# Performance work log

Measured on AMD Instinct MI355X. Metric: run time of the kernel, lower is better.

## Reference

```python
import jax, jax.numpy as jnp
import numpy as np

B, NJ, NM = 64, 30, 20
N = NJ * NM          # 600 operation nodes per FJSP instance
IN_DIM, H = 2, 128


def _bn(h):
    # torch BatchNorm1d in training mode, gamma=1/beta=0 (module init), stats over all nodes
    m = h.mean(axis=(0, 1))
    v = h.var(axis=(0, 1))
    return (h - m) / jnp.sqrt(v + 1e-5)


def setup_inputs() -> dict:
    key = jax.random.key(0)
    ks = jax.random.split(key, 20)
    x = jax.random.normal(ks[0], (B, N, IN_DIM), jnp.float32)
    graph_pool = jnp.full((B, N), 1.0 / N, jnp.float32)   # average graph pooling weights
    padded_nei = jnp.zeros((1,), jnp.int32)               # unused (sum pooling path)
    adj = (jax.random.uniform(ks[1], (B, N, N)) < 0.01).astype(jnp.float32)
    adj = jnp.minimum(adj + jnp.eye(N, dtype=jnp.float32)[None], 1.0)  # self-loops
    candidate = jax.random.randint(ks[2], (B, NJ), 0, N)
    a_index = jax.random.randint(ks[3], (B,), 0, NJ)
    mask = jax.random.uniform(ks[4], (B, NJ)) < 0.2
    mask = mask.at[jnp.arange(B), a_index].set(False)     # chosen action never masked
    mask_mch = jax.random.uniform(ks[5], (B, N, NM)) < 0.3
    dur = jax.random.uniform(ks[6], (B, N, NM), dtype=jnp.float32)
    old_action = jax.random.randint(ks[7], (B,), 0, N)
    mch_pool = jax.random.normal(ks[8], (B, H), jnp.float32)

    def w(k, i, o):
        return jax.random.normal(k, (i, o), jnp.float32) * (1.0 / np.sqrt(i))

    z = lambda n: jnp.zeros((n,), jnp.float32)            # biases init to 0 in module
    return dict(
        x=x, graph_pool=graph_pool, padded_nei=padded_nei, adj=adj,
        candidate=candidate, mask=mask, mask_mch=mask_mch, dur=dur,
        a_index=a_index, old_action=old_action, mch_pool=mch_pool,
        W1_0=w(ks[9], IN_DIM, H), b1_0=z(H), W2_0=w(ks[10], H, H), b2_0=z(H),
        W1_1=w(ks[11], H, H), b1_1=z(H), W2_1=w(ks[12], H, H), b2_1=z(H),
        Wa1=w(ks[13], 3 * H, H), ba1=z(H), Wa2=w(ks[14], H, H), ba2=z(H),
        Wa3=w(ks[15], H, 1), ba3=z(1),
        Wc1=w(ks[16], H, H), bc1=z(H), Wc2=w(ks[17], H, 1), bc2=z(1),
    )


def reference(x, graph_pool, padded_nei, adj, candidate, mask, mask_mch, dur,
              a_index, old_action, mch_pool,
              W1_0, b1_0, W2_0, b2_0, W1_1, b1_1, W2_1, b2_1,
              Wa1, ba1, Wa2, ba2, Wa3, ba3, Wc1, bc1, Wc2, bc2):
    # --- GIN encoder: num_layers-1 = 2 message-passing layers, sum pooling ---
    h = x
    for (W1, b1, W2, b2) in ((W1_0, b1_0, W2_0, b2_0), (W1_1, b1_1, W2_1, b2_1)):
        pooled = jnp.einsum('bnm,bmd->bnd', adj, h)         # neighbor sum (adj has self-loops)
        h1 = jax.nn.relu(_bn(pooled @ W1 + b1))             # MLP hidden (BN inside MLP)
        h = jax.nn.relu(_bn(h1 @ W2 + b2))                  # layer BN + relu
    h_nodes = h                                             # [B, N, H]
    h_pooled = jnp.einsum('bn,bnd->bd', graph_pool, h_nodes)  # [B, H]

    # --- gather candidate features, concat pooled contexts ---
    cand_feat = jnp.take_along_axis(h_nodes, candidate[:, :, None], axis=1)  # [B, NJ, H]
    concat = jnp.concatenate([
        cand_feat,
        jnp.broadcast_to(h_pooled[:, None, :], cand_feat.shape),
        jnp.broadcast_to(mch_pool[:, None, :], cand_feat.shape)], axis=-1)   # [B, NJ, 3H]

    # --- MLPActor(3 layers, tanh) ---
    a = jnp.tanh(concat @ Wa1 + ba1)
    a = jnp.tanh(a @ Wa2 + ba2)
    scores = (a @ Wa3 + ba3).squeeze(-1) * 10.0             # [B, NJ]
    scores = jnp.where(mask, -jnp.inf, scores)
    logpi = jax.nn.log_softmax(scores, axis=1)
    pi = jnp.exp(logpi)
    log_a = jnp.take_along_axis(logpi, a_index[:, None], axis=1)[:, 0]
    entropy = -jnp.sum(jnp.where(pi > 0, pi * logpi, 0.0), axis=1)

    # --- gather action-dependent tensors (detached in torch) ---
    b_idx = jnp.arange(B)
    action_node = dur[b_idx, old_action]                    # [B, NM]
    action_feature = h_nodes[b_idx, old_action]             # [B, H]
    mask_mch_action = mask_mch[b_idx, old_action][:, None, :]  # [B, 1, NM]

    # --- MLPCritic(2 layers, tanh) ---
    v = jnp.tanh(h_pooled @ Wc1 + bc1) @ Wc2 + bc2          # [B, 1]

    sg = jax.lax.stop_gradient
    return (entropy, v, log_a, sg(action_node), sg(action_feature),
            mask_mch_action, sg(h_pooled))
```

## Files before the change

### kernel.cpp

```cpp
#include <hip/hip_runtime.h>
#include <hip/hip_bf16.h>

#define BB 64
#define NJ 30
#define NM 20
#define NN 600
#define HH 128
#define NROWS (BB*NN)
#define CAP 48

typedef __attribute__((ext_vector_type(8))) short short8;
typedef __attribute__((ext_vector_type(4))) float f32x4;

#define STATS_B   0
#define HPOOL_B   4096
#define FLAGS_B   36864
#define ZERO_B    36880
#define WTB_B     37120
#define SCORES_B  135424
#define NBRCNT_B  143104
#define NBRIDX_B  296704
#define POOLED0_B 7669504
#define T1_B      7976704
#define P1_B      27637504

#define OUT_ENT   0
#define OUT_V     64
#define OUT_LOGA  128
#define OUT_ANODE 192
#define OUT_AFEAT 1472
#define OUT_MMCH  9664
#define OUT_HPOOL 10944

__device__ __forceinline__ bool mask_at(const void* p, int layout, long i) {
    if (layout == 2) return ((const float*)p)[i] != 0.f;
    if (layout == 1) return ((const unsigned char*)p)[i] != 0;
    return ((const int*)p)[i] != 0;
}

__device__ __forceinline__ short bf16rne(float f) {
    unsigned u = __float_as_uint(f);
    return (short)((u + 0x7fffu + ((u >> 16) & 1u)) >> 16);
}
__device__ __forceinline__ float bf2f(unsigned h) {
    return __uint_as_float(h << 16);
}
__device__ __forceinline__ unsigned packbf(float a, float b) {
    return ((unsigned)(unsigned short)bf16rne(a)) |
           (((unsigned)(unsigned short)bf16rne(b)) << 16);
}

__global__ __launch_bounds__(256) void k_sparse(const float* __restrict__ adj,
                                                const float* __restrict__ x,
                                                int* __restrict__ nbr_cnt,
                                                int* __restrict__ nbr_idx,
                                                float* __restrict__ pooled0,
                                                const void* mask_p, const void* maskmch_p,
                                                int* flags,
                                                const float* __restrict__ Wa,
                                                const float* __restrict__ Wb,
                                                const float* __restrict__ Wc,
                                                unsigned short* __restrict__ wT) {
    int bid = blockIdx.x;
    int tid = threadIdx.x;
    if (bid < 289) {
        if (bid >= 97) {
            int bid2 = bid - 97;
            int mat = bid2 >> 6;
            int idx = ((bid2 & 63) << 8) + tid;
            const float* W = mat == 0 ? Wa : (mat == 1 ? Wb : Wc);
            int k = idx >> 7, c = idx & 127;
            wT[mat * 16384 + c * HH + k] = (unsigned short)bf16rne(W[idx]);
        } else {
            unsigned agg = 0;
            int which;
            if (bid == 0) {
                which = 0;
                const unsigned* p = (const unsigned*)mask_p;
                unsigned w0 = (tid < 480) ? p[tid] : 0u;
                unsigned w1 = (tid + 256 < 480) ? p[tid + 256] : 0u;
                agg = w0 | w1;
            } else {
                which = 1;
                const unsigned* p = (const unsigned*)maskmch_p + (size_t)(bid - 1) * 200;
                agg = (tid < 200) ? p[tid] : 0u;
            }
            int f = 0;
            if (((agg >> 24) & 0xffu) == 0x3fu) f |= 1;
            if ((((agg >> 8) & 0xffu) == 1u) || (((agg >> 16) & 0xffu) == 1u) ||
                (((agg >> 24) & 0xffu) == 1u)) f |= 2;
#pragma unroll
            for (int off = 1; off < 64; off <<= 1) f |= __shfl_xor(f, off);
            if ((tid & 63) == 0 && f) atomicOr(&flags[which], f);
        }
    }

    int wrow = bid * 4 + (tid >> 6);
    int lane = tid & 63;
    int b = wrow / NN;
    const float4* arow = (const float4*)(adj + (size_t)wrow * NN);
    int* irow = nbr_idx + (size_t)wrow * CAP;
    const float* xb = x + (size_t)b * NN * 2;
    float4 vv[3];
    vv[0] = arow[lane];
    vv[1] = arow[64 + lane];
    vv[2] = (128 + lane < 150) ? arow[128 + lane] : make_float4(0.f, 0.f, 0.f, 0.f);
    int cnt = 0;
    float p0 = 0.f, p1 = 0.f;
#pragma unroll
    for (int it = 0; it < 3; ++it) {
        float4 v = vv[it];
        int col0 = it * 256 + lane * 4;
        bool m0 = v.x != 0.f, m1 = v.y != 0.f, m2 = v.z != 0.f, m3 = v.w != 0.f;
        int c_lane = (int)m0 + (int)m1 + (int)m2 + (int)m3;
        int inc = c_lane;
#pragma unroll
        for (int off = 1; off < 64; off <<= 1) {
            int t = __shfl_up(inc, off);
            if (lane >= off) inc += t;
        }
        int pos = cnt + inc - c_lane;
        if (m0) {
            if (pos < CAP) irow[pos] = col0;
            float2 xv = *(const float2*)&xb[col0 * 2];
            p0 += xv.x; p1 += xv.y; ++pos;
        }
        if (m1) {
            if (pos < CAP) irow[pos] = col0 + 1;
            float2 xv = *(const float2*)&xb[(col0 + 1) * 2];
            p0 += xv.x; p1 += xv.y; ++pos;
        }
        if (m2) {
            if (pos < CAP) irow[pos] = col0 + 2;
            float2 xv = *(const float2*)&xb[(col0 + 2) * 2];
            p0 += xv.x; p1 += xv.y; ++pos;
        }
        if (m3) {
            if (pos < CAP) irow[pos] = col0 + 3;
            float2 xv = *(const float2*)&xb[(col0 + 3) * 2];
            p0 += xv.x; p1 += xv.y; ++pos;
        }
        cnt += __shfl(inc, 63);
    }
#pragma unroll
    for (int off = 1; off < 64; off <<= 1) {
        p0 += __shfl_xor(p0, off);
        p1 += __shfl_xor(p1, off);
    }
    if (lane == 0) {
        nbr_cnt[wrow] = cnt < CAP ? cnt : CAP;
        pooled0[(size_t)wrow * 2]     = p0;
        pooled0[(size_t)wrow * 2 + 1] = p1;
    }
}

__global__ __launch_bounds__(256) void k_p0stats(const float* __restrict__ pooled0,
                                                 float* __restrict__ out5) {
    __shared__ float red[4][5];
    int i = blockIdx.x * 256 + threadIdx.x;
    float p0 = pooled0[(size_t)i * 2], p1 = pooled0[(size_t)i * 2 + 1];
    float v[5] = {p0, p1, p0 * p0, p1 * p1, p0 * p1};
#pragma unroll
    for (int j = 0; j < 5; ++j)
#pragma unroll
        for (int off = 1; off < 64; off <<= 1) v[j] += __shfl_xor(v[j], off);
    int lane = threadIdx.x & 63, w = threadIdx.x >> 6;
    if (lane == 0)
#pragma unroll
        for (int j = 0; j < 5; ++j) red[w][j] = v[j];
    __syncthreads();
    if (threadIdx.x == 0)
#pragma unroll
        for (int j = 0; j < 5; ++j)
            atomicAdd(&out5[j], red[0][j] + red[1][j] + red[2][j] + red[3][j]);
}

template<int MODE>
__global__ __launch_bounds__(256) void k_stage(const void* __restrict__ t_in_v,
                                               const float* __restrict__ pooled0,
                                               const float* __restrict__ W1,
                                               const unsigned short* __restrict__ wT,
                                               const float* __restrict__ stats_in,
                                               unsigned short* __restrict__ t_out,
                                               float* __restrict__ stats_out) {
    __shared__ float sm_mean[HH], sm_inv[HH];
    __shared__ float smS[4][32], smQ[4][32];
    int tid = threadIdx.x;
    if (MODE == 0 && tid < HH) {
        float S0 = stats_in[0], S1 = stats_in[1], Q0 = stats_in[2], Q1 = stats_in[3], P01 = stats_in[4];
        float w0 = W1[tid], w1 = W1[HH + tid];
        float m = (S0 * w0 + S1 * w1) * (1.f / NROWS);
        float eq = (Q0 * w0 * w0 + Q1 * w1 * w1 + 2.f * P01 * w0 * w1) * (1.f / NROWS);
        sm_mean[tid] = m;
        sm_inv[tid] = 1.f / sqrtf(eq - m * m + 1e-5f);
    }
    if (MODE == 1 && tid < HH) {
        float s = stats_in[tid], q = stats_in[HH + tid];
        float m = s * (1.f / NROWS);
        sm_mean[tid] = m;
        sm_inv[tid] = 1.f / sqrtf(q * (1.f / NROWS) - m * m + 1e-5f);
    }
    if (MODE != 2) __syncthreads();

    const unsigned short* tin = (const unsigned short*)t_in_v;
    int lane = tid & 63, wave = tid >> 6;
    int r16 = lane & 15, kg = lane >> 4;
    int rowbase = (blockIdx.x >> 2) * 64 + wave * 16;
    int colq = blockIdx.x & 3;

    f32x4 acc[2];
#pragma unroll
    for (int t = 0; t < 2; ++t)
#pragma unroll
        for (int i = 0; i < 4; ++i) acc[t][i] = 0.f;

    float p0 = 0.f, p1 = 0.f;
    if (MODE == 0) {
        p0 = pooled0[(size_t)(rowbase + r16) * 2];
        p1 = pooled0[(size_t)(rowbase + r16) * 2 + 1];
    }

#pragma unroll
    for (int ks = 0; ks < 4; ++ks) {
        int kb = ks * 32 + kg * 8;
        short8 afr;
        if (MODE == 2) {
            afr = *(const short8*)&tin[(size_t)(rowbase + r16) * HH + kb];
        } else {
            float av[8];
            if (MODE == 0) {
                float4 wa0 = *(const float4*)&W1[kb];
                float4 wa1 = *(const float4*)&W1[kb + 4];
                float4 wb0 = *(const float4*)&W1[HH + kb];
                float4 wb1 = *(const float4*)&W1[HH + kb + 4];
                av[0] = p0 * wa0.x + p1 * wb0.x; av[1] = p0 * wa0.y + p1 * wb0.y;
                av[2] = p0 * wa0.z + p1 * wb0.z; av[3] = p0 * wa0.w + p1 * wb0.w;
                av[4] = p0 * wa1.x + p1 * wb1.x; av[5] = p0 * wa1.y + p1 * wb1.y;
                av[6] = p0 * wa1.z + p1 * wb1.z; av[7] = p0 * wa1.w + p1 * wb1.w;
            } else {
                short8 raw = *(const short8*)&tin[(size_t)(rowbase + r16) * HH + kb];
#pragma unroll
                for (int j = 0; j < 8; ++j) av[j] = bf2f((unsigned short)raw[j]);
            }
            float4 m0 = *(const float4*)&sm_mean[kb];
            float4 m1 = *(const float4*)&sm_mean[kb + 4];
            float4 i0 = *(const float4*)&sm_inv[kb];
            float4 i1 = *(const float4*)&sm_inv[kb + 4];
            av[0] = fmaxf((av[0] - m0.x) * i0.x, 0.f);
            av[1] = fmaxf((av[1] - m0.y) * i0.y, 0.f);
            av[2] = fmaxf((av[2] - m0.z) * i0.z, 0.f);
            av[3] = fmaxf((av[3] - m0.w) * i0.w, 0.f);
            av[4] = fmaxf((av[4] - m1.x) * i1.x, 0.f);
            av[5] = fmaxf((av[5] - m1.y) * i1.y, 0.f);
            av[6] = fmaxf((av[6] - m1.z) * i1.z, 0.f);
            av[7] = fmaxf((av[7] - m1.w) * i1.w, 0.f);
#pragma unroll
            for (int j = 0; j < 8; ++j) afr[j] = bf16rne(av[j]);
        }
#pragma unroll
        for (int t = 0; t < 2; ++t) {
            short8 bfr = *(const short8*)&wT[(size_t)((colq * 2 + t) * 16 + r16) * HH + kb];
            acc[t] = __builtin_amdgcn_mfma_f32_16x16x32_bf16(afr, bfr, acc[t], 0, 0, 0);
        }
    }

#pragma unroll
    for (int t = 0; t < 2; ++t) {
        int lc = t * 16 + r16;
        int col = colq * 32 + lc;
        float s = 0.f, q = 0.f;
#pragma unroll
        for (int i = 0; i < 4; ++i) {
            float v = acc[t][i];
            t_out[(size_t)(rowbase + kg * 4 + i) * HH + col] = (unsigned short)bf16rne(v);
            s += v; q += v * v;
        }
        s += __shfl_xor(s, 16); q += __shfl_xor(q, 16);
        s += __shfl_xor(s, 32); q += __shfl_xor(q, 32);
        if (kg == 0) { smS[wave][lc] = s; smQ[wave][lc] = q; }
    }
    __syncthreads();
    if (tid < 32) {
        int col = colq * 32 + tid;
        atomicAdd(&stats_out[col],      smS[0][tid] + smS[1][tid] + smS[2][tid] + smS[3][tid]);
        atomicAdd(&stats_out[HH + col], smQ[0][tid] + smQ[1][tid] + smQ[2][tid] + smQ[3][tid]);
    }
}

__global__ __launch_bounds__(256) void k_pool1(const unsigned short* __restrict__ t1,
                                               const int* __restrict__ nbr_cnt,
                                               const int* __restrict__ nbr_idx,
                                               const float* __restrict__ stats1,
                                               unsigned short* __restrict__ pooled1) {
    __shared__ float sm_mean[HH], sm_inv[HH];
    int tid = threadIdx.x;
    if (tid < HH) {
        float s = stats1[tid], q = stats1[HH + tid];
        float m = s * (1.f / NROWS);
        sm_mean[tid] = m;
        sm_inv[tid] = 1.f / sqrtf(q * (1.f / NROWS) - m * m + 1e-5f);
    }
    __syncthreads();
    int c4 = tid & 31, rl = tid >> 5;
    int row = blockIdx.x * 8 + rl;
    int b = row / NN;
    float4 mm = *(const float4*)&sm_mean[c4 * 4];
    float4 iv = *(const float4*)&sm_inv[c4 * 4];
    int cnt = nbr_cnt[row];
    const int* ir = nbr_idx + (size_t)row * CAP;
    const unsigned short* tb = t1 + (size_t)b * NN * HH;
    float a0 = 0.f, a1 = 0.f, a2 = 0.f, a3 = 0.f;
    int i = 0;
    for (; i + 1 < cnt; i += 2) {
        int m0 = ir[i], m1 = ir[i + 1];
        uint2 w0 = *(const uint2*)&tb[(size_t)m0 * HH + c4 * 4];
        uint2 w1 = *(const uint2*)&tb[(size_t)m1 * HH + c4 * 4];
        a0 += fmaxf((bf2f(w0.x & 0xffffu) - mm.x) * iv.x, 0.f)
            + fmaxf((bf2f(w1.x & 0xffffu) - mm.x) * iv.x, 0.f);
        a1 += fmaxf((bf2f(w0.x >> 16)     - mm.y) * iv.y, 0.f)
            + fmaxf((bf2f(w1.x >> 16)     - mm.y) * iv.y, 0.f);
        a2 += fmaxf((bf2f(w0.y & 0xffffu) - mm.z) * iv.z, 0.f)
            + fmaxf((bf2f(w1.y & 0xffffu) - mm.z) * iv.z, 0.f);
        a3 += fmaxf((bf2f(w0.y >> 16)     - mm.w) * iv.w, 0.f)
            + fmaxf((bf2f(w1.y >> 16)     - mm.w) * iv.w, 0.f);
    }
    if (i < cnt) {
        int m0 = ir[i];
        uint2 w0 = *(const uint2*)&tb[(size_t)m0 * HH + c4 * 4];
        a0 += fmaxf((bf2f(w0.x & 0xffffu) - mm.x) * iv.x, 0.f);
        a1 += fmaxf((bf2f(w0.x >> 16)     - mm.y) * iv.y, 0.f);
        a2 += fmaxf((bf2f(w0.y & 0xffffu) - mm.z) * iv.z, 0.f);
        a3 += fmaxf((bf2f(w0.y >> 16)     - mm.w) * iv.w, 0.f);
    }
    uint2 o;
    o.x = packbf(a0, a1);
    o.y = packbf(a2, a3);
    *(uint2*)&pooled1[(size_t)row * HH + c4 * 4] = o;
}

__global__ __launch_bounds__(256) void k_hpool(const unsigned short* __restrict__ t3,
                                               const float* __restrict__ gp,
                                               const float* __restrict__ stats3,
                                               float* __restrict__ hpool) {
    __shared__ float sm_mean[HH], sm_inv[HH];
    __shared__ float red[8][HH];
    int tid = threadIdx.x;
    if (tid < HH) {
        float s = stats3[tid], q = stats3[HH + tid];
        float m = s * (1.f / NROWS);
        sm_mean[tid] = m;
        sm_inv[tid] = 1.f / sqrtf(q * (1.f / NROWS) - m * m + 1e-5f);
    }
    __syncthreads();
    int b = blockIdx.x >> 3, chunk = blockIdx.x & 7;
    int c4 = tid & 31, rl = tid >> 5;
    float4 mm = *(const float4*)&sm_mean[c4 * 4];
    float4 iv = *(const float4*)&sm_inv[c4 * 4];
    float a0 = 0.f, a1 = 0.f, a2 = 0.f, a3 = 0.f;
    int nend = chunk * 75 + 75;
    for (int n = chunk * 75 + rl; n < nend; n += 8) {
        float w = gp[b * NN + n];
        uint2 t = *(const uint2*)&t3[((size_t)b * NN + n) * HH + c4 * 4];
        a0 += w * fmaxf((bf2f(t.x & 0xffffu) - mm.x) * iv.x, 0.f);
        a1 += w * fmaxf((bf2f(t.x >> 16)     - mm.y) * iv.y, 0.f);
        a2 += w * fmaxf((bf2f(t.y & 0xffffu) - mm.z) * iv.z, 0.f);
        a3 += w * fmaxf((bf2f(t.y >> 16)     - mm.w) * iv.w, 0.f);
    }
    *(float4*)&red[rl][c4 * 4] = make_float4(a0, a1, a2, a3);
    __syncthreads();
    if (tid < HH) {
        float s = 0.f;
#pragma unroll
        for (int g = 0; g < 8; ++g) s += red[g][tid];
        atomicAdd(&hpool[b * HH + tid], s);
    }
}

__global__ __launch_bounds__(256) void k_actor(const unsigned short* __restrict__ t3,
                                               const int* __restrict__ cand,
                                               const float* __restrict__ hpool,
                                               const float* __restrict__ mch,
                                               const float* __restrict__ stats3,
                                               const float* __restrict__ Wa1,
                                               const float* __restrict__ ba1,
                                               const float* __restrict__ Wa2,
                                               const float* __restrict__ ba2,
                                               const float* __restrict__ Wa3,
                                               const float* __restrict__ ba3,
                                               float* __restrict__ scores) {
    __shared__ float sh_c[8 * 384];
    __shared__ float sh_a1[8 * HH];
    __shared__ float sred[8][HH];
    int tid = threadIdx.x;
    int rbase = blockIdx.x * 8;
    int c = tid & 127, slot = tid >> 7;

    float mean_c, inv_c;
    {
        float s = stats3[c], q = stats3[HH + c];
        float m = s * (1.f / NROWS);
        mean_c = m;
        inv_c = 1.f / sqrtf(q * (1.f / NROWS) - m * m + 1e-5f);
    }
#pragma unroll
    for (int rr = 0; rr < 4; ++rr) {
        int r = slot * 4 + rr;
        int row = rbase + r;
        int b = row / NJ;
        int cd = cand[row];
        float v = bf2f(t3[((size_t)b * NN + cd) * HH + c]);
        sh_c[r * 384 + c]       = fmaxf((v - mean_c) * inv_c, 0.f);
        sh_c[r * 384 + 128 + c] = hpool[b * HH + c];
        sh_c[r * 384 + 256 + c] = mch[b * HH + c];
    }
    __syncthreads();

    float acc[4] = {0.f, 0.f, 0.f, 0.f};
    for (int k = 0; k < 384; ++k) {
        float w = Wa1[(size_t)k * HH + c];
#pragma unroll
        for (int rr = 0; rr < 4; ++rr)
            acc[rr] += sh_c[(slot * 4 + rr) * 384 + k] * w;
    }
    float bb = ba1[c];
#pragma unroll
    for (int rr = 0; rr < 4; ++rr)
        sh_a1[(slot * 4 + rr) * HH + c] = tanhf(acc[rr] + bb);
    __syncthreads();

    float acc2[4] = {0.f, 0.f, 0.f, 0.f};
    for (int k = 0; k < HH; ++k) {
        float w = Wa2[(size_t)k * HH + c];
#pragma unroll
        for (int rr = 0; rr < 4; ++rr)
            acc2[rr] += sh_a1[(slot * 4 + rr) * HH + k] * w;
    }
    float w3 = Wa3[c], bb2 = ba2[c];
#pragma unroll
    for (int rr = 0; rr < 4; ++rr)
        sred[slot * 4 + rr][c] = tanhf(acc2[rr] + bb2) * w3;
    __syncthreads();
    int r = tid >> 5, l32 = tid & 31;
    float v = sred[r][l32] + sred[r][l32 + 32] + sred[r][l32 + 64] + sred[r][l32 + 96];
    v += __shfl_xor(v, 1); v += __shfl_xor(v, 2); v += __shfl_xor(v, 4);
    v += __shfl_xor(v, 8); v += __shfl_xor(v, 16);
    if (l32 == 0) scores[rbase + r] = 10.f * (v + ba3[0]);
}

__global__ __launch_bounds__(128) void k_final(const unsigned short* __restrict__ t3,
                                               const float* __restrict__ stats3,
                                               const float* __restrict__ hpool,
                                               const float* __restrict__ scores,
                                               const void* __restrict__ mask_p,
                                               const void* __restrict__ maskmch_p,
                                               const int* __restrict__ flags,
                                               const float* __restrict__ dur,
                                               const int* __restrict__ a_index,
                                               const int* __restrict__ old_action,
                                               const float* __restrict__ Wc1,
                                               const float* __restrict__ bc1,
                                               const float* __restrict__ Wc2,
                                               const float* __restrict__ bc2,
                                               float* __restrict__ out) {
    __shared__ float sm_mean[HH], sm_inv[HH], sh_hp[HH], sh_red[HH];
    __shared__ float sh_s[32], sh_lp[32];
    __shared__ int sh_m[32];
    int b = blockIdx.x, t = threadIdx.x;
    {
        float s = stats3[t], q = stats3[HH + t];
        float m = s * (1.f / NROWS);
        sm_mean[t] = m;
        sm_inv[t] = 1.f / sqrtf(q * (1.f / NROWS) - m * m + 1e-5f);
    }
    sh_hp[t] = hpool[b * HH + t];
    __syncthreads();

    float acc = bc1[t];
    for (int k = 0; k < HH; ++k) acc += sh_hp[k] * Wc1[k * HH + t];
    sh_red[t] = tanhf(acc) * Wc2[t];
    __syncthreads();
    for (int st = 64; st > 0; st >>= 1) {
        if (t < st) sh_red[t] += sh_red[t + st];
        __syncthreads();
    }
    if (t == 0) out[OUT_V + b] = sh_red[0] + bc2[0];

    int fA = flags[0], fB = flags[1];
    int layA = (fA & 1) ? 2 : ((fA & 2) ? 1 : 0);
    int layB = (fB & 1) ? 2 : ((fB & 2) ? 1 : 0);
    if (t < NJ) {
        sh_s[t] = scores[b * NJ + t];
        sh_m[t] = mask_at(mask_p, layA, (long)b * NJ + t) ? 1 : 0;
    }
    __syncthreads();
    if (t == 0) {
        float mx = -1e30f;
        for (int j = 0; j < NJ; ++j)
            if (!sh_m[j] && sh_s[j] > mx) mx = sh_s[j];
        float sum = 0.f;
        for (int j = 0; j < NJ; ++j)
            if (!sh_m[j]) sum += expf(sh_s[j] - mx);
        float lse = mx + logf(sum);
        float ent = 0.f;
        for (int j = 0; j < NJ; ++j) {
            if (!sh_m[j]) {
                float lp = sh_s[j] - lse;
                sh_lp[j] = lp;
                float pi = expf(lp);
                if (pi > 0.f) ent -= pi * lp;
            }
        }
        out[OUT_ENT + b] = ent;
        out[OUT_LOGA + b] = sh_lp[a_index[b]];
    }

    int old = old_action[b];
    if (t < NM) {
        out[OUT_ANODE + b * NM + t] = dur[((size_t)b * NN + old) * NM + t];
        out[OUT_MMCH + b * NM + t] =
            mask_at(maskmch_p, layB, ((size_t)b * NN + old) * NM + t) ? 1.f : 0.f;
    }
    {
        float v = bf2f(t3[((size_t)b * NN + old) * HH + t]);
        out[OUT_AFEAT + b * HH + t] = fmaxf((v - sm_mean[t]) * sm_inv[t], 0.f);
        out[OUT_HPOOL + b * HH + t] = sh_hp[t];
    }
}

extern "C" void kernel_launch(void* const* d_in, const int* in_sizes, int n_in,
                              void* d_out, int out_size, void* d_ws, size_t ws_size,
                              hipStream_t stream) {
    (void)in_sizes; (void)n_in; (void)out_size; (void)ws_size;
    const float* x         = (const float*)d_in[0];
    const float* gp        = (const float*)d_in[1];
    const float* adj       = (const float*)d_in[3];
    const int*   cand      = (const int*)d_in[4];
    const void*  mask_p    = d_in[5];
    const void*  maskmch_p = d_in[6];
    const float* dur       = (const float*)d_in[7];
    const int*   a_index   = (const int*)d_in[8];
    const int*   old_act   = (const int*)d_in[9];
    const float* mch_pool  = (const float*)d_in[10];
    const float* W1_0 = (const float*)d_in[11];
    const float* W2_0 = (const float*)d_in[13];
    const float* W1_1 = (const float*)d_in[15];
    const float* W2_1 = (const float*)d_in[17];
    const float* Wa1  = (const float*)d_in[19];
    const float* ba1  = (const float*)d_in[20];
    const float* Wa2  = (const float*)d_in[21];
    const float* ba2  = (const float*)d_in[22];
    const float* Wa3  = (const float*)d_in[23];
    const float* ba3  = (const float*)d_in[24];
    const float* Wc1  = (const float*)d_in[25];
    const float* bc1  = (const float*)d_in[26];
    const float* Wc2  = (const float*)d_in[27];
    const float* bc2  = (const float*)d_in[28];

    char* ws = (char*)d_ws;
    float* stats   = (float*)(ws + STATS_B);
    float* hpool   = (float*)(ws + HPOOL_B);
    int*   flags   = (int*)(ws + FLAGS_B);
    unsigned short* wtb = (unsigned short*)(ws + WTB_B);
    float* scores  = (float*)(ws + SCORES_B);
    int*   nbr_cnt = (int*)(ws + NBRCNT_B);
    int*   nbr_idx = (int*)(ws + NBRIDX_B);
    float* pooled0 = (float*)(ws + POOLED0_B);
    unsigned short* t1_16 = (unsigned short*)(ws + T1_B);
    unsigned short* p1_16 = (unsigned short*)(ws + P1_B);
    float* out     = (float*)d_out;

    hipMemsetAsync(ws, 0, ZERO_B, stream);
    k_sparse<<<NROWS / 4, 256, 0, stream>>>(adj, x, nbr_cnt, nbr_idx, pooled0,
                                            mask_p, maskmch_p, flags, W2_0, W1_1, W2_1, wtb);
    k_p0stats<<<NROWS / 256, 256, 0, stream>>>(pooled0, stats);
    k_stage<0><<<2400, 256, 0, stream>>>(nullptr, pooled0, W1_0, wtb, stats, t1_16, stats + 256);
    k_pool1<<<NROWS / 8, 256, 0, stream>>>(t1_16, nbr_cnt, nbr_idx, stats + 256, p1_16);
    k_stage<2><<<2400, 256, 0, stream>>>(p1_16, nullptr, nullptr, wtb + 16384, stats, t1_16, stats + 512);
    k_stage<1><<<2400, 256, 0, stream>>>(t1_16, nullptr, nullptr, wtb + 32768, stats + 512,
                                         p1_16, stats + 768);
    k_hpool<<<BB * 8, 256, 0, stream>>>(p1_16, gp, stats + 768, hpool);
    k_actor<<<240, 256, 0, stream>>>(p1_16, cand, hpool, mch_pool, stats + 768,
                                     Wa1, ba1, Wa2, ba2, Wa3, ba3, scores);
    k_final<<<BB, 128, 0, stream>>>(p1_16, stats + 768, hpool, scores, mask_p, maskmch_p, flags,
                                    dur, a_index, old_act, Wc1, bc1, Wc2, bc2, out);
}
```

Before: 352.5 us.

## Fuse pooled-input stats into sparse kernel and merge tail kernels into one

```diff
diff --git a/kernel.cpp b/kernel.cpp
--- a/kernel.cpp
+++ b/kernel.cpp
@@ -60,7 +60,9 @@
                                                 const float* __restrict__ Wa,
                                                 const float* __restrict__ Wb,
                                                 const float* __restrict__ Wc,
-                                                unsigned short* __restrict__ wT) {
+                                                unsigned short* __restrict__ wT,
+                                                float* __restrict__ stats5) {
+    __shared__ float sst[4][5];
     int bid = blockIdx.x;
     int tid = threadIdx.x;
     if (bid < 289) {
@@ -97,6 +99,7 @@
 
     int wrow = bid * 4 + (tid >> 6);
     int lane = tid & 63;
+    int wave = tid >> 6;
     int b = wrow / NN;
     const float4* arow = (const float4*)(adj + (size_t)wrow * NN);
     int* irow = nbr_idx + (size_t)wrow * CAP;
@@ -151,28 +154,13 @@
         nbr_cnt[wrow] = cnt < CAP ? cnt : CAP;
         pooled0[(size_t)wrow * 2]     = p0;
         pooled0[(size_t)wrow * 2 + 1] = p1;
-    }
-}
-
-__global__ __launch_bounds__(256) void k_p0stats(const float* __restrict__ pooled0,
-                                                 float* __restrict__ out5) {
-    __shared__ float red[4][5];
-    int i = blockIdx.x * 256 + threadIdx.x;
-    float p0 = pooled0[(size_t)i * 2], p1 = pooled0[(size_t)i * 2 + 1];
-    float v[5] = {p0, p1, p0 * p0, p1 * p1, p0 * p1};
-#pragma unroll
-    for (int j = 0; j < 5; ++j)
-#pragma unroll
-        for (int off = 1; off < 64; off <<= 1) v[j] += __shfl_xor(v[j], off);
-    int lane = threadIdx.x & 63, w = threadIdx.x >> 6;
-    if (lane == 0)
-#pragma unroll
-        for (int j = 0; j < 5; ++j) red[w][j] = v[j];
-    __syncthreads();
-    if (threadIdx.x == 0)
-#pragma unroll
-        for (int j = 0; j < 5; ++j)
-            atomicAdd(&out5[j], red[0][j] + red[1][j] + red[2][j] + red[3][j]);
+        sst[wave][0] = p0; sst[wave][1] = p1;
+        sst[wave][2] = p0 * p0; sst[wave][3] = p1 * p1; sst[wave][4] = p0 * p1;
+    }
+    __syncthreads();
+    if (tid < 5)
+        atomicAdd(&stats5[(bid & 7) * 5 + tid],
+                  sst[0][tid] + sst[1][tid] + sst[2][tid] + sst[3][tid]);
 }
 
 template<int MODE>
@@ -187,7 +175,15 @@
     __shared__ float smS[4][32], smQ[4][32];
     int tid = threadIdx.x;
     if (MODE == 0 && tid < HH) {
-        float S0 = stats_in[0], S1 = stats_in[1], Q0 = stats_in[2], Q1 = stats_in[3], P01 = stats_in[4];
+        float S0 = 0.f, S1 = 0.f, Q0 = 0.f, Q1 = 0.f, P01 = 0.f;
+#pragma unroll
+        for (int g = 0; g < 8; ++g) {
+            S0  += stats_in[g * 5 + 0];
+            S1  += stats_in[g * 5 + 1];
+            Q0  += stats_in[g * 5 + 2];
+            Q1  += stats_in[g * 5 + 3];
+            P01 += stats_in[g * 5 + 4];
+        }
         float w0 = W1[tid], w1 = W1[HH + tid];
         float m = (S0 * w0 + S1 * w1) * (1.f / NROWS);
         float eq = (Q0 * w0 * w0 + Q1 * w1 * w1 + 2.f * P01 * w0 * w1) * (1.f / NROWS);
@@ -338,13 +334,39 @@
     *(uint2*)&pooled1[(size_t)row * HH + c4 * 4] = o;
 }
 
-__global__ __launch_bounds__(256) void k_hpool(const unsigned short* __restrict__ t3,
-                                               const float* __restrict__ gp,
-                                               const float* __restrict__ stats3,
-                                               float* __restrict__ hpool) {
+__global__ __launch_bounds__(256) void k_tail(const unsigned short* __restrict__ t3,
+                                              const float* __restrict__ gp,
+                                              const int* __restrict__ cand,
+                                              const float* __restrict__ mch,
+                                              const float* __restrict__ stats3,
+                                              const void* __restrict__ mask_p,
+                                              const void* __restrict__ maskmch_p,
+                                              const int* __restrict__ flags,
+                                              const float* __restrict__ dur,
+                                              const int* __restrict__ a_index,
+                                              const int* __restrict__ old_action,
+                                              const float* __restrict__ Wa1,
+                                              const float* __restrict__ ba1,
+                                              const float* __restrict__ Wa2,
+                                              const float* __restrict__ ba2,
+                                              const float* __restrict__ Wa3,
+                                              const float* __restrict__ ba3,
+                                              const float* __restrict__ Wc1,
+                                              const float* __restrict__ bc1,
+                                              const float* __restrict__ Wc2,
+                                              const float* __restrict__ bc2,
+                                              float* __restrict__ out) {
     __shared__ float sm_mean[HH], sm_inv[HH];
     __shared__ float red[8][HH];
-    int tid = threadIdx.x;
+    __shared__ float sh_hp[HH];
+    __shared__ float sh_base[HH];
+    __shared__ float sh_cand[NJ][HH];
+    __shared__ float sh_a1[NJ][HH];
+    __shared__ float sred[NJ][HH];
+    __shared__ float sh_s[32], sh_lp[32];
+    __shared__ int sh_m[32];
+
+    int b = blockIdx.x, tid = threadIdx.x;
     if (tid < HH) {
         float s = stats3[tid], q = stats3[HH + tid];
         float m = s * (1.f / NROWS);
@@ -352,148 +374,116 @@
         sm_inv[tid] = 1.f / sqrtf(q * (1.f / NROWS) - m * m + 1e-5f);
     }
     __syncthreads();
-    int b = blockIdx.x >> 3, chunk = blockIdx.x & 7;
-    int c4 = tid & 31, rl = tid >> 5;
-    float4 mm = *(const float4*)&sm_mean[c4 * 4];
-    float4 iv = *(const float4*)&sm_inv[c4 * 4];
-    float a0 = 0.f, a1 = 0.f, a2 = 0.f, a3 = 0.f;
-    int nend = chunk * 75 + 75;
-    for (int n = chunk * 75 + rl; n < nend; n += 8) {
-        float w = gp[b * NN + n];
-        uint2 t = *(const uint2*)&t3[((size_t)b * NN + n) * HH + c4 * 4];
-        a0 += w * fmaxf((bf2f(t.x & 0xffffu) - mm.x) * iv.x, 0.f);
-        a1 += w * fmaxf((bf2f(t.x >> 16)     - mm.y) * iv.y, 0.f);
-        a2 += w * fmaxf((bf2f(t.y & 0xffffu) - mm.z) * iv.z, 0.f);
-        a3 += w * fmaxf((bf2f(t.y >> 16)     - mm.w) * iv.w, 0.f);
-    }
-    *(float4*)&red[rl][c4 * 4] = make_float4(a0, a1, a2, a3);
+
+    {
+        int c4 = tid & 31, rl = tid >> 5;
+        float4 mm = *(const float4*)&sm_mean[c4 * 4];
+        float4 iv = *(const float4*)&sm_inv[c4 * 4];
+        float a0 = 0.f, a1 = 0.f, a2 = 0.f, a3 = 0.f;
+        for (int n = rl; n < NN; n += 8) {
+            float w = gp[b * NN + n];
+            uint2 t = *(const uint2*)&t3[((size_t)b * NN + n) * HH + c4 * 4];
+            a0 += w * fmaxf((bf2f(t.x & 0xffffu) - mm.x) * iv.x, 0.f);
+            a1 += w * fmaxf((bf2f(t.x >> 16)     - mm.y) * iv.y, 0.f);
+            a2 += w * fmaxf((bf2f(t.y & 0xffffu) - mm.z) * iv.z, 0.f);
+            a3 += w * fmaxf((bf2f(t.y >> 16)     - mm.w) * iv.w, 0.f);
+        }
+        *(float4*)&red[rl][c4 * 4] = make_float4(a0, a1, a2, a3);
+    }
     __syncthreads();
     if (tid < HH) {
         float s = 0.f;
 #pragma unroll
         for (int g = 0; g < 8; ++g) s += red[g][tid];
-        atomicAdd(&hpool[b * HH + tid], s);
-    }
-}
-
-__global__ __launch_bounds__(256) void k_actor(const unsigned short* __restrict__ t3,
-                                               const int* __restrict__ cand,
-                                               const float* __restrict__ hpool,
-                                               const float* __restrict__ mch,
-                                               const float* __restrict__ stats3,
-                                               const float* __restrict__ Wa1,
-                                               const float* __restrict__ ba1,
-                                               const float* __restrict__ Wa2,
-                                               const float* __restrict__ ba2,
-                                               const float* __restrict__ Wa3,
-                                               const float* __restrict__ ba3,
-                                               float* __restrict__ scores) {
-    __shared__ float sh_c[8 * 384];
-    __shared__ float sh_a1[8 * HH];
-    __shared__ float sred[8][HH];
-    int tid = threadIdx.x;
-    int rbase = blockIdx.x * 8;
-    int c = tid & 127, slot = tid >> 7;
-
-    float mean_c, inv_c;
+        sh_hp[tid] = s;
+        out[OUT_HPOOL + b * HH + tid] = s;
+    }
+    __syncthreads();
+
     {
-        float s = stats3[c], q = stats3[HH + c];
-        float m = s * (1.f / NROWS);
-        mean_c = m;
-        inv_c = 1.f / sqrtf(q * (1.f / NROWS) - m * m + 1e-5f);
-    }
-#pragma unroll
-    for (int rr = 0; rr < 4; ++rr) {
-        int r = slot * 4 + rr;
-        int row = rbase + r;
-        int b = row / NJ;
-        int cd = cand[row];
-        float v = bf2f(t3[((size_t)b * NN + cd) * HH + c]);
-        sh_c[r * 384 + c]       = fmaxf((v - mean_c) * inv_c, 0.f);
-        sh_c[r * 384 + 128 + c] = hpool[b * HH + c];
-        sh_c[r * 384 + 256 + c] = mch[b * HH + c];
-    }
-    __syncthreads();
-
-    float acc[4] = {0.f, 0.f, 0.f, 0.f};
-    for (int k = 0; k < 384; ++k) {
-        float w = Wa1[(size_t)k * HH + c];
-#pragma unroll
-        for (int rr = 0; rr < 4; ++rr)
-            acc[rr] += sh_c[(slot * 4 + rr) * 384 + k] * w;
-    }
-    float bb = ba1[c];
-#pragma unroll
-    for (int rr = 0; rr < 4; ++rr)
-        sh_a1[(slot * 4 + rr) * HH + c] = tanhf(acc[rr] + bb);
-    __syncthreads();
-
-    float acc2[4] = {0.f, 0.f, 0.f, 0.f};
-    for (int k = 0; k < HH; ++k) {
-        float w = Wa2[(size_t)k * HH + c];
-#pragma unroll
-        for (int rr = 0; rr < 4; ++rr)
-            acc2[rr] += sh_a1[(slot * 4 + rr) * HH + k] * w;
-    }
-    float w3 = Wa3[c], bb2 = ba2[c];
-#pragma unroll
-    for (int rr = 0; rr < 4; ++rr)
-        sred[slot * 4 + rr][c] = tanhf(acc2[rr] + bb2) * w3;
-    __syncthreads();
-    int r = tid >> 5, l32 = tid & 31;
-    float v = sred[r][l32] + sred[r][l32 + 32] + sred[r][l32 + 64] + sred[r][l32 + 96];
-    v += __shfl_xor(v, 1); v += __shfl_xor(v, 2); v += __shfl_xor(v, 4);
-    v += __shfl_xor(v, 8); v += __shfl_xor(v, 16);
-    if (l32 == 0) scores[rbase + r] = 10.f * (v + ba3[0]);
-}
-
-__global__ __launch_bounds__(128) void k_final(const unsigned short* __restrict__ t3,
-                                               const float* __restrict__ stats3,
-                                               const float* __restrict__ hpool,
-                                               const float* __restrict__ scores,
-                                               const void* __restrict__ mask_p,
-                                               const void* __restrict__ maskmch_p,
-                                               const int* __restrict__ flags,
-                                               const float* __restrict__ dur,
-                                               const int* __restrict__ a_index,
-                                               const int* __restrict__ old_action,
-                                               const float* __restrict__ Wc1,
-                                               const float* __restrict__ bc1,
-                                               const float* __restrict__ Wc2,
-                                               const float* __restrict__ bc2,
-                                               float* __restrict__ out) {
-    __shared__ float sm_mean[HH], sm_inv[HH], sh_hp[HH], sh_red[HH];
-    __shared__ float sh_s[32], sh_lp[32];
-    __shared__ int sh_m[32];
-    int b = blockIdx.x, t = threadIdx.x;
+        int c = tid & 127, slot = tid >> 7;
+        float acc = 0.f;
+        if (slot == 0) {
+            for (int k = 0; k < HH; ++k)
+                acc += sh_hp[k] * Wa1[(size_t)(HH + k) * HH + c];
+        } else {
+            const float* mb = mch + b * HH;
+            for (int k = 0; k < HH; ++k)
+                acc += mb[k] * Wa1[(size_t)(2 * HH + k) * HH + c];
+        }
+        red[slot][c] = acc;
+        for (int j = slot; j < NJ; j += 2) {
+            int cd = cand[b * NJ + j];
+            float v = bf2f(t3[((size_t)b * NN + cd) * HH + c]);
+            sh_cand[j][c] = fmaxf((v - sm_mean[c]) * sm_inv[c], 0.f);
+        }
+    }
+    __syncthreads();
+    if (tid < HH) sh_base[tid] = red[0][tid] + red[1][tid] + ba1[tid];
+    __syncthreads();
+
     {
-        float s = stats3[t], q = stats3[HH + t];
-        float m = s * (1.f / NROWS);
-        sm_mean[t] = m;
-        sm_inv[t] = 1.f / sqrtf(q * (1.f / NROWS) - m * m + 1e-5f);
-    }
-    sh_hp[t] = hpool[b * HH + t];
-    __syncthreads();
-
-    float acc = bc1[t];
-    for (int k = 0; k < HH; ++k) acc += sh_hp[k] * Wc1[k * HH + t];
-    sh_red[t] = tanhf(acc) * Wc2[t];
+        int c = tid & 127, slot = tid >> 7;
+        float acc[15];
+#pragma unroll
+        for (int r = 0; r < 15; ++r) acc[r] = 0.f;
+        for (int k = 0; k < HH; ++k) {
+            float w = Wa1[(size_t)k * HH + c];
+#pragma unroll
+            for (int r = 0; r < 15; ++r)
+                acc[r] += sh_cand[slot * 15 + r][k] * w;
+        }
+        float bb = sh_base[c];
+#pragma unroll
+        for (int r = 0; r < 15; ++r)
+            sh_a1[slot * 15 + r][c] = tanhf(acc[r] + bb);
+    }
+    __syncthreads();
+
+    {
+        int c = tid & 127, slot = tid >> 7;
+        float acc[15];
+#pragma unroll
+        for (int r = 0; r < 15; ++r) acc[r] = 0.f;
+        for (int k = 0; k < HH; ++k) {
+            float w = Wa2[(size_t)k * HH + c];
+#pragma unroll
+            for (int r = 0; r < 15; ++r)
+                acc[r] += sh_a1[slot * 15 + r][k] * w;
+        }
+        float w3 = Wa3[c], bb2 = ba2[c];
+#pragma unroll
+        for (int r = 0; r < 15; ++r)
+            sred[slot * 15 + r][c] = tanhf(acc[r] + bb2) * w3;
+    }
+    __syncthreads();
+
+    {
+        int wv = tid >> 6, l = tid & 63;
+        for (int r = wv; r < NJ; r += 4) {
+            float v = sred[r][l] + sred[r][l + 64];
+            v += __shfl_xor(v, 1); v += __shfl_xor(v, 2); v += __shfl_xor(v, 4);
+            v += __shfl_xor(v, 8); v += __shfl_xor(v, 16); v += __shfl_xor(v, 32);
+            if (l == 0) sh_s[r] = 10.f * (v + ba3[0]);
+        }
+    }
+
+    if (tid < HH) {
+        float acc = bc1[tid];
+        for (int k = 0; k < HH; ++k) acc += sh_hp[k] * Wc1[k * HH + tid];
+        red[0][tid] = tanhf(acc) * Wc2[tid];
+    }
+    if (tid < NJ)
+        sh_m[tid] = mask_at(mask_p, ((flags[0] & 1) ? 2 : ((flags[0] & 2) ? 1 : 0)),
+                            (long)b * NJ + tid) ? 1 : 0;
     __syncthreads();
     for (int st = 64; st > 0; st >>= 1) {
-        if (t < st) sh_red[t] += sh_red[t + st];
+        if (tid < st) red[0][tid] += red[0][tid + st];
         __syncthreads();
     }
-    if (t == 0) out[OUT_V + b] = sh_red[0] + bc2[0];
-
-    int fA = flags[0], fB = flags[1];
-    int layA = (fA & 1) ? 2 : ((fA & 2) ? 1 : 0);
-    int layB = (fB & 1) ? 2 : ((fB & 2) ? 1 : 0);
-    if (t < NJ) {
-        sh_s[t] = scores[b * NJ + t];
-        sh_m[t] = mask_at(mask_p, layA, (long)b * NJ + t) ? 1 : 0;
-    }
-    __syncthreads();
-    if (t == 0) {
+    if (tid == 0) out[OUT_V + b] = red[0][0] + bc2[0];
+
+    if (tid == 0) {
         float mx = -1e30f;
         for (int j = 0; j < NJ; ++j)
             if (!sh_m[j] && sh_s[j] > mx) mx = sh_s[j];
@@ -514,16 +504,19 @@
         out[OUT_LOGA + b] = sh_lp[a_index[b]];
     }
 
-    int old = old_action[b];
-    if (t < NM) {
-        out[OUT_ANODE + b * NM + t] = dur[((size_t)b * NN + old) * NM + t];
-        out[OUT_MMCH + b * NM + t] =
-            mask_at(maskmch_p, layB, ((size_t)b * NN + old) * NM + t) ? 1.f : 0.f;
-    }
     {
-        float v = bf2f(t3[((size_t)b * NN + old) * HH + t]);
-        out[OUT_AFEAT + b * HH + t] = fmaxf((v - sm_mean[t]) * sm_inv[t], 0.f);
-        out[OUT_HPOOL + b * HH + t] = sh_hp[t];
+        int old = old_action[b];
+        int fB = flags[1];
+        int layB = (fB & 1) ? 2 : ((fB & 2) ? 1 : 0);
+        if (tid < NM) {
+            out[OUT_ANODE + b * NM + tid] = dur[((size_t)b * NN + old) * NM + tid];
+            out[OUT_MMCH + b * NM + tid] =
+                mask_at(maskmch_p, layB, ((size_t)b * NN + old) * NM + tid) ? 1.f : 0.f;
+        }
+        if (tid < HH) {
+            float v = bf2f(t3[((size_t)b * NN + old) * HH + tid]);
+            out[OUT_AFEAT + b * HH + tid] = fmaxf((v - sm_mean[tid]) * sm_inv[tid], 0.f);
+        }
     }
 }
 
@@ -558,10 +551,8 @@
 
     char* ws = (char*)d_ws;
     float* stats   = (float*)(ws + STATS_B);
-    float* hpool   = (float*)(ws + HPOOL_B);
     int*   flags   = (int*)(ws + FLAGS_B);
     unsigned short* wtb = (unsigned short*)(ws + WTB_B);
-    float* scores  = (float*)(ws + SCORES_B);
     int*   nbr_cnt = (int*)(ws + NBRCNT_B);
     int*   nbr_idx = (int*)(ws + NBRIDX_B);
     float* pooled0 = (float*)(ws + POOLED0_B);
@@ -571,16 +562,16 @@
 
     hipMemsetAsync(ws, 0, ZERO_B, stream);
     k_sparse<<<NROWS / 4, 256, 0, stream>>>(adj, x, nbr_cnt, nbr_idx, pooled0,
-                                            mask_p, maskmch_p, flags, W2_0, W1_1, W2_1, wtb);
-    k_p0stats<<<NROWS / 256, 256, 0, stream>>>(pooled0, stats);
+                                            mask_p, maskmch_p, flags, W2_0, W1_1, W2_1,
+                                            wtb, stats);
     k_stage<0><<<2400, 256, 0, stream>>>(nullptr, pooled0, W1_0, wtb, stats, t1_16, stats + 256);
     k_pool1<<<NROWS / 8, 256, 0, stream>>>(t1_16, nbr_cnt, nbr_idx, stats + 256, p1_16);
-    k_stage<2><<<2400, 256, 0, stream>>>(p1_16, nullptr, nullptr, wtb + 16384, stats, t1_16, stats + 512);
+    k_stage<2><<<2400, 256, 0, stream>>>(p1_16, nullptr, nullptr, wtb + 16384, nullptr,
+                                         t1_16, stats + 512);
     k_stage<1><<<2400, 256, 0, stream>>>(t1_16, nullptr, nullptr, wtb + 32768, stats + 512,
                                          p1_16, stats + 768);
-    k_hpool<<<BB * 8, 256, 0, stream>>>(p1_16, gp, stats + 768, hpool);
-    k_actor<<<240, 256, 0, stream>>>(p1_16, cand, hpool, mch_pool, stats + 768,
-                                     Wa1, ba1, Wa2, ba2, Wa3, ba3, scores);
-    k_final<<<BB, 128, 0, stream>>>(p1_16, stats + 768, hpool, scores, mask_p, maskmch_p, flags,
-                                    dur, a_index, old_act, Wc1, bc1, Wc2, bc2, out);
-}
+    k_tail<<<BB, 256, 0, stream>>>(p1_16, gp, cand, mch_pool, stats + 768,
+                                   mask_p, maskmch_p, flags, dur, a_index, old_act,
+                                   Wa1, ba1, Wa2, ba2, Wa3, ba3,
+                                   Wc1, bc1, Wc2, bc2, out);
+}
```

After: 418.9 us. +18.8%, slower.
